# Kernel tuning notes

Measured on AMD Instinct MI355X. Metric: run time of the kernel, lower is better.

Reference implementation:

```python
import jax, jax.numpy as jnp
import numpy as np
from jax import lax

NEG = -1e9  # finite stand-in for -inf (keeps gradients NaN-free)
EPS = 1e-7  # keras.backend.epsilon()


def _logadd3(a, b, c):
    m = jnp.maximum(jnp.maximum(a, b), c)
    return m + jnp.log(jnp.exp(a - m) + jnp.exp(b - m) + jnp.exp(c - m))


def setup_inputs() -> dict:
    key = jax.random.key(0)
    k1, k2, k3, k4 = jax.random.split(key, 4)
    B, T, V, L = 32, 1000, 1024, 100
    logits = jax.random.normal(k1, (B, T, V), dtype=jnp.float32)
    predictions = jax.nn.softmax(logits, axis=-1)  # ctc_batch_cost expects probabilities
    labels = jax.random.randint(k2, (B, L), 0, V - 1, dtype=jnp.int32)  # blank=V-1 excluded
    input_lengths = jax.random.randint(k3, (B, 1), T // 2, T + 1, dtype=jnp.int32)
    label_lengths = jax.random.randint(k4, (B, 1), L // 2, L + 1, dtype=jnp.int32)
    return {"predictions": predictions, "input_lengths": input_lengths,
            "labels": labels, "label_lengths": label_lengths}


def _ctc_loss(predictions, input_lengths, labels, label_lengths):
    B, T, V = predictions.shape
    L = labels.shape[1]
    S = 2 * L + 1
    blank = V - 1

    log_probs = jnp.log(predictions + EPS)  # [B,T,V]

    # Extended label sequence: blank interleaved -> [B,S]
    ext = jnp.full((B, S), blank, dtype=jnp.int32).at[:, 1::2].set(labels)
    ext_m2 = jnp.concatenate([jnp.full((B, 2), -1, jnp.int32), ext[:, :-2]], axis=1)
    allow_skip = (ext != blank) & (ext != ext_m2)  # [B,S]

    s_idx = jnp.arange(S)[None, :]
    valid = s_idx < (2 * label_lengths + 1)  # [B,S] mask of reachable DP lanes

    # Emission log-probs along the extended sequence: [B,T,S]
    emit = jnp.take_along_axis(log_probs, jnp.broadcast_to(ext[:, None, :], (B, T, S)), axis=2)

    alpha0 = jnp.full((B, S), NEG, dtype=log_probs.dtype)
    alpha0 = alpha0.at[:, 0].set(emit[:, 0, 0]).at[:, 1].set(emit[:, 0, 1])
    alpha0 = jnp.where(valid, alpha0, NEG)

    neg1 = jnp.full((B, 1), NEG, dtype=log_probs.dtype)
    neg2 = jnp.full((B, 2), NEG, dtype=log_probs.dtype)

    def step(alpha, xs):
        emit_t, t = xs
        a = alpha
        b = jnp.concatenate([neg1, alpha[:, :-1]], axis=1)
        c = jnp.where(allow_skip, jnp.concatenate([neg2, alpha[:, :-2]], axis=1), NEG)
        new = jnp.where(valid, _logadd3(a, b, c) + emit_t, NEG)
        alpha = jnp.where(t < input_lengths, new, alpha)  # freeze past input_length
        return alpha, None

    emits = jnp.swapaxes(emit, 0, 1)[1:]  # [T-1,B,S]
    ts = jnp.arange(1, T)
    alpha_final, _ = lax.scan(step, alpha0, (emits, ts))

    a_lab = jnp.take_along_axis(alpha_final, 2 * label_lengths - 1, axis=1)  # last label
    a_blk = jnp.take_along_axis(alpha_final, 2 * label_lengths, axis=1)      # trailing blank
    loglik = jnp.logaddexp(a_lab, a_blk)  # [B,1]
    return -loglik


def reference(predictions, input_lengths, labels, label_lengths):
    per_utt = _ctc_loss(predictions, input_lengths, labels, label_lengths)  # [B,1]
    return jnp.mean(per_utt)
```

## Files before the change

kernel.cpp:

```cpp
#include <hip/hip_runtime.h>

#define EPSF  (1e-7f)
#define LN2F  (0.69314718055994530942f)

constexpr int Tc = 1000;
constexpr int Vc = 1024;
constexpr int Lc = 100;
constexpr int GW = 128;
constexpr int CH = 32;

#define SHFLUP1Z(x) __int_as_float(__builtin_amdgcn_update_dpp( \
        0, __float_as_int(x), 0x138, 0xF, 0xF, false))

#define DPPMAXSTEP(x, ctrl) \
    x = fmaxf(x, __int_as_float(__builtin_amdgcn_update_dpp( \
        0, __float_as_int(x), ctrl, 0xF, 0xF, true)))

__global__ __launch_bounds__(128) void ctc_gather_kernel(
    const float* __restrict__ pred,
    const int*   __restrict__ labels,
    const int*   __restrict__ ilen,
    float*       __restrict__ E)
{
    const int row = blockIdx.x;
    const int j   = threadIdx.x;
    const int b   = row / Tc;
    const int t   = row - b * Tc;
    if (t >= ilen[b]) return;
    const int* lab = labels + b * Lc;
    int col = -1;
    if (j < 64) {
        if (j < 50)       col = lab[2 * j];
        else if (j == 50) col = Vc - 1;
    } else {
        int k = j - 64;
        if (k < 50)       col = lab[2 * k + 1];
    }
    float v = 0.0f;
    if (col >= 0) v = pred[(size_t)row * Vc + col] + EPSF;
    E[(size_t)row * GW + j] = v;
}

__global__ __launch_bounds__(64) void ctc_dp_kernel(
    const float* __restrict__ E,
    const int*   __restrict__ ilen,
    const int*   __restrict__ labels,
    const int*   __restrict__ llen,
    float*       __restrict__ loss)
{
    const int b = blockIdx.x;
    const int l = threadIdx.x;

    const int il = ilen[b];
    const int ll = llen[b];
    const int Tb = min(Tc, il);

    const int* lab = labels + b * Lc;
    const int lab0 = lab[min(2 * l,     Lc - 1)];
    const int lab1 = lab[min(2 * l + 1, Lc - 1)];
    const int labm = lab[max(2 * l - 1, 0)];
    const bool allow1 = (l == 0) || (lab0 != labm);
    const bool allow3 = (lab1 != lab0);

    const int Sv = 2 * ll + 1;
    const bool valid0 = (4 * l + 0) < Sv;
    const bool valid1 = (4 * l + 1) < Sv;
    const bool valid2 = (4 * l + 2) < Sv;
    const bool valid3 = (4 * l + 3) < Sv;

    const float* Eb = E + (size_t)b * Tc * GW;

    __shared__ float lds[2][CH][GW];
    __shared__ float sh[256];

    float a0 = 0.0f, a1 = 0.0f, a2 = 0.0f, a3 = 0.0f;
    if (l == 0) { a0 = Eb[50]; a1 = Eb[0]; }
    int Eshift = 0;

#define STEP(Lb, r) do {                                                      \
        float e0_ = (Lb)[(r) * GW + l];                                       \
        float e1_ = (Lb)[(r) * GW + 64 + l];                                  \
        float eb_ = (Lb)[(r) * GW + 50];                                      \
        float p3s_ = SHFLUP1Z(a3);                                            \
        float p2s_ = SHFLUP1Z(a2);                                            \
        float n0_ = (a0 + p3s_) * eb_;                                        \
        float c1_ = allow1 ? p2s_ : 0.0f;                                     \
        float n1_ = (a1 + a0 + c1_) * e0_;                                    \
        float n2_ = (a2 + a1) * eb_;                                          \
        float c3_ = allow3 ? a1 : 0.0f;                                       \
        float n3_ = (a3 + a2 + c3_) * e1_;                                    \
        a0 = valid0 ? n0_ : 0.0f;                                             \
        a1 = valid1 ? n1_ : 0.0f;                                             \
        a2 = valid2 ? n2_ : 0.0f;                                             \
        a3 = valid3 ? n3_ : 0.0f;                                             \
    } while (0)

#define RESCALE() do {                                                        \
        float m_ = fmaxf(fmaxf(a0, a1), fmaxf(a2, a3));                       \
        DPPMAXSTEP(m_, 0x111);                                \
        DPPMAXSTEP(m_, 0x112);                                \
        DPPMAXSTEP(m_, 0x114);                                \
        DPPMAXSTEP(m_, 0x118);                                \
        DPPMAXSTEP(m_, 0x142);                              \
        DPPMAXSTEP(m_, 0x143);                              \
        int mb_ = __builtin_amdgcn_readlane(__float_as_int(m_), 63);          \
        int Ee_ = (mb_ >> 23) & 0xFF;                                         \
        float sc_ = __int_as_float((253 - Ee_) << 23);        \
        a0 *= sc_; a1 *= sc_; a2 *= sc_; a3 *= sc_;                           \
        Eshift += Ee_ - 126;                                                  \
    } while (0)

#define LOADCHUNK(t0n_) do {                                                  \
        _Pragma("unroll")                                                     \
        for (int p_ = 0; p_ < 16; ++p_) {                                     \
            int r0_ = min((t0n_) + 2 * p_, Tc - 2);                           \
            g[p_] = *(const float4*)(Eb + (size_t)r0_ * GW + 4 * l);          \
        }                                                                     \
    } while (0)

#define WRITECHUNK(buf_) do {                                                 \
        float* d_ = &lds[buf_][0][0] + 4 * l;                                 \
        _Pragma("unroll")                                                     \
        for (int p_ = 0; p_ < 16; ++p_) {                                     \
            *(float4*)(d_ + p_ * 2 * GW) = g[p_];                             \
        }                                                                     \
    } while (0)

    float4 g[16];

    LOADCHUNK(0);
    __builtin_amdgcn_sched_barrier(0);
    WRITECHUNK(0);
    int buf = 0;

    {
        const bool pf = (CH < Tb);
        if (pf) LOADCHUNK(CH);
        __builtin_amdgcn_sched_barrier(0);
        const float* Lb = &lds[0][0][0];
#pragma unroll
        for (int k = 1; k < 8; ++k) STEP(Lb, k);
        RESCALE();
#pragma unroll
        for (int gi = 1; gi < 4; ++gi) {
#pragma unroll
            for (int k = 0; k < 8; ++k) STEP(Lb, gi * 8 + k);
            RESCALE();
        }
        if (pf) WRITECHUNK(1);
        buf = 1;
    }

    for (int t0 = CH; t0 < Tb; t0 += CH) {
        const int t0n = t0 + CH;
        const bool pf = (t0n < Tb);
        if (pf) LOADCHUNK(t0n);
        __builtin_amdgcn_sched_barrier(0);
        const float* Lb = &lds[buf][0][0];
        const int ns = min(CH, Tb - t0);
        if (ns == CH) {
#pragma unroll
            for (int gi = 0; gi < 4; ++gi) {
#pragma unroll
                for (int k = 0; k < 8; ++k) STEP(Lb, gi * 8 + k);
                RESCALE();
            }
        } else {
            for (int r = 0; r < ns; ++r) {
                STEP(Lb, r);
                if ((r & 7) == 7) RESCALE();
            }
        }
        if (pf) WRITECHUNK(buf ^ 1);
        buf ^= 1;
    }
#undef STEP
#undef RESCALE
#undef LOADCHUNK
#undef WRITECHUNK

    sh[4 * l + 0] = a0; sh[4 * l + 1] = a1;
    sh[4 * l + 2] = a2; sh[4 * l + 3] = a3;
    __syncthreads();
    if (l == 0) {
        float x = sh[2 * ll - 1], y = sh[2 * ll];
        loss[b] = -(__logf(x + y) + (float)Eshift * LN2F);
    }
}

__global__ void ctc_reduce_kernel(const float* __restrict__ loss,
                                  float* __restrict__ out, int B)
{
    int lane = threadIdx.x;
    float x = (lane < B) ? loss[lane] : 0.0f;
#pragma unroll
    for (int off = 32; off > 0; off >>= 1)
        x += __shfl_down(x, off);
    if (lane == 0) out[0] = x / (float)B;
}

extern "C" void kernel_launch(void* const* d_in, const int* in_sizes, int n_in,
                              void* d_out, int out_size, void* d_ws, size_t ws_size,
                              hipStream_t stream)
{
    const float* pred   = (const float*)d_in[0];
    const int*   ilen   = (const int*)d_in[1];
    const int*   labels = (const int*)d_in[2];
    const int*   llen   = (const int*)d_in[3];
    float*       out    = (float*)d_out;
    float*       wsloss = (float*)d_ws;
    float*       Ebuf   = (float*)((char*)d_ws + 256);

    const int B = in_sizes[1];

    ctc_gather_kernel<<<B * Tc, 128, 0, stream>>>(pred, labels, ilen, Ebuf);
    ctc_dp_kernel<<<B, 64, 0, stream>>>(Ebuf, ilen, labels, llen, wsloss);
    ctc_reduce_kernel<<<1, 64, 0, stream>>>(wsloss, out, B);
}
```

Baseline: 270.3 us.

## Prefetch DP emissions into registers and fold validity masks into gather

The DP kernel no longer stages emission rows through a double-buffered LDS chunk. Each lane now loads its own emission values directly from global memory into register arrays, grouped eight rows at a time and issued 32 time steps ahead of use. The per-step validity selects are removed: the gather kernel writes zero emissions for label lanes beyond the label length, so unreachable states stay at zero on their own. The skip gating becomes an FMA with a 0/1 multiplier. This removes LDS writes, reads and per-step selects from the serial recurrence, at the cost of higher register use and reliance on global load latency being hidden by the prefetch distance.

```diff
diff --git a/kernel.cpp b/kernel.cpp
--- a/kernel.cpp
+++ b/kernel.cpp
@@ -7,7 +7,6 @@
 constexpr int Vc = 1024;
 constexpr int Lc = 100;
 constexpr int GW = 128;
-constexpr int CH = 32;
 
 #define SHFLUP1Z(x) __int_as_float(__builtin_amdgcn_update_dpp( \
         0, __float_as_int(x), 0x138, 0xF, 0xF, false))
@@ -20,6 +19,7 @@
     const float* __restrict__ pred,
     const int*   __restrict__ labels,
     const int*   __restrict__ ilen,
+    const int*   __restrict__ llen,
     float*       __restrict__ E)
 {
     const int row = blockIdx.x;
@@ -27,17 +27,20 @@
     const int b   = row / Tc;
     const int t   = row - b * Tc;
     if (t >= ilen[b]) return;
+    const int ll = llen[b];
     const int* lab = labels + b * Lc;
-    int col = -1;
+    float v = 0.0f;
     if (j < 64) {
-        if (j < 50)       col = lab[2 * j];
-        else if (j == 50) col = Vc - 1;
+        if (j < 50) {
+            if (2 * j < ll) v = pred[(size_t)row * Vc + lab[2 * j]] + EPSF;
+        } else if (j == 50) {
+            v = pred[(size_t)row * Vc + (Vc - 1)] + EPSF;
+        }
     } else {
         int k = j - 64;
-        if (k < 50)       col = lab[2 * k + 1];
-    }
-    float v = 0.0f;
-    if (col >= 0) v = pred[(size_t)row * Vc + col] + EPSF;
+        if (k < 50 && (2 * k + 1) < ll)
+            v = pred[(size_t)row * Vc + lab[2 * k + 1]] + EPSF;
+    }
     E[(size_t)row * GW + j] = v;
 }
 
@@ -59,40 +62,52 @@
     const int lab0 = lab[min(2 * l,     Lc - 1)];
     const int lab1 = lab[min(2 * l + 1, Lc - 1)];
     const int labm = lab[max(2 * l - 1, 0)];
-    const bool allow1 = (l == 0) || (lab0 != labm);
-    const bool allow3 = (lab1 != lab0);
-
-    const int Sv = 2 * ll + 1;
-    const bool valid0 = (4 * l + 0) < Sv;
-    const bool valid1 = (4 * l + 1) < Sv;
-    const bool valid2 = (4 * l + 2) < Sv;
-    const bool valid3 = (4 * l + 3) < Sv;
+    const float allow1f = ((l == 0) || (lab0 != labm)) ? 1.0f : 0.0f;
+    const float allow3f = (lab1 != lab0) ? 1.0f : 0.0f;
 
     const float* Eb = E + (size_t)b * Tc * GW;
 
-    __shared__ float lds[2][CH][GW];
     __shared__ float sh[256];
 
     float a0 = 0.0f, a1 = 0.0f, a2 = 0.0f, a3 = 0.0f;
     if (l == 0) { a0 = Eb[50]; a1 = Eb[0]; }
     int Eshift = 0;
 
-#define STEP(Lb, r) do {                                                      \
-        float e0_ = (Lb)[(r) * GW + l];                                       \
-        float e1_ = (Lb)[(r) * GW + 64 + l];                                  \
-        float eb_ = (Lb)[(r) * GW + 50];                                      \
+    float v0[32], v1[32], vb[32];
+
+#define LOADG(gi, baseRow) do {                                               \
+        const int br_ = (baseRow);                                            \
+        if (br_ + 7 <= Tc - 1) {                                              \
+            const float* p_ = Eb + (size_t)br_ * GW;                          \
+            _Pragma("unroll")                                                 \
+            for (int k_ = 0; k_ < 8; ++k_) {                                  \
+                v0[8 * (gi) + k_] = p_[k_ * GW + l];                          \
+                v1[8 * (gi) + k_] = p_[k_ * GW + 64 + l];                     \
+                vb[8 * (gi) + k_] = p_[k_ * GW + 50];                         \
+            }                                                                 \
+        } else {                                                              \
+            _Pragma("unroll")                                                 \
+            for (int k_ = 0; k_ < 8; ++k_) {                                  \
+                int r_ = min(br_ + k_, Tc - 1);    \
+                const float* p_ = Eb + (size_t)r_ * GW;                       \
+                v0[8 * (gi) + k_] = p_[l];                                    \
+                v1[8 * (gi) + k_] = p_[64 + l];                               \
+                vb[8 * (gi) + k_] = p_[50];                                   \
+            }                                                                 \
+        }                                                                     \
+    } while (0)
+
+#define STEP(gi, k) do {                                                      \
+        float e0_ = v0[8 * (gi) + (k)];                                       \
+        float e1_ = v1[8 * (gi) + (k)];                                       \
+        float eb_ = vb[8 * (gi) + (k)];                                       \
         float p3s_ = SHFLUP1Z(a3);                                            \
         float p2s_ = SHFLUP1Z(a2);                                            \
         float n0_ = (a0 + p3s_) * eb_;                                        \
-        float c1_ = allow1 ? p2s_ : 0.0f;                                     \
-        float n1_ = (a1 + a0 + c1_) * e0_;                                    \
+        float n1_ = fmaf(p2s_, allow1f, a1 + a0) * e0_;                       \
         float n2_ = (a2 + a1) * eb_;                                          \
-        float c3_ = allow3 ? a1 : 0.0f;                                       \
-        float n3_ = (a3 + a2 + c3_) * e1_;                                    \
-        a0 = valid0 ? n0_ : 0.0f;                                             \
-        a1 = valid1 ? n1_ : 0.0f;                                             \
-        a2 = valid2 ? n2_ : 0.0f;                                             \
-        a3 = valid3 ? n3_ : 0.0f;                                             \
+        float n3_ = fmaf(a1, allow3f, a3 + a2) * e1_;                         \
+        a0 = n0_; a1 = n1_; a2 = n2_; a3 = n3_;                               \
     } while (0)
 
 #define RESCALE() do {                                                        \
@@ -110,74 +125,44 @@
         Eshift += Ee_ - 126;                                                  \
     } while (0)
 
-#define LOADCHUNK(t0n_) do {                                                  \
-        _Pragma("unroll")                                                     \
-        for (int p_ = 0; p_ < 16; ++p_) {                                     \
-            int r0_ = min((t0n_) + 2 * p_, Tc - 2);                           \
-            g[p_] = *(const float4*)(Eb + (size_t)r0_ * GW + 4 * l);          \
-        }                                                                     \
-    } while (0)
-
-#define WRITECHUNK(buf_) do {                                                 \
-        float* d_ = &lds[buf_][0][0] + 4 * l;                                 \
-        _Pragma("unroll")                                                     \
-        for (int p_ = 0; p_ < 16; ++p_) {                                     \
-            *(float4*)(d_ + p_ * 2 * GW) = g[p_];                             \
-        }                                                                     \
-    } while (0)
-
-    float4 g[16];
-
-    LOADCHUNK(0);
-    __builtin_amdgcn_sched_barrier(0);
-    WRITECHUNK(0);
-    int buf = 0;
-
-    {
-        const bool pf = (CH < Tb);
-        if (pf) LOADCHUNK(CH);
-        __builtin_amdgcn_sched_barrier(0);
-        const float* Lb = &lds[0][0][0];
-#pragma unroll
-        for (int k = 1; k < 8; ++k) STEP(Lb, k);
-        RESCALE();
-#pragma unroll
-        for (int gi = 1; gi < 4; ++gi) {
-#pragma unroll
-            for (int k = 0; k < 8; ++k) STEP(Lb, gi * 8 + k);
-            RESCALE();
+    LOADG(0, 1); LOADG(1, 9); LOADG(2, 17); LOADG(3, 25);
+
+    int t0 = 1;
+    for (; t0 + 32 <= Tb; t0 += 32) {
+        __builtin_amdgcn_sched_barrier(0);
+#pragma unroll
+        for (int k = 0; k < 8; ++k) STEP(0, k);
+        RESCALE();
+        LOADG(0, t0 + 32);
+        __builtin_amdgcn_sched_barrier(0);
+#pragma unroll
+        for (int k = 0; k < 8; ++k) STEP(1, k);
+        RESCALE();
+        LOADG(1, t0 + 40);
+        __builtin_amdgcn_sched_barrier(0);
+#pragma unroll
+        for (int k = 0; k < 8; ++k) STEP(2, k);
+        RESCALE();
+        LOADG(2, t0 + 48);
+        __builtin_amdgcn_sched_barrier(0);
+#pragma unroll
+        for (int k = 0; k < 8; ++k) STEP(3, k);
+        RESCALE();
+        LOADG(3, t0 + 56);
+    }
+
+#pragma unroll
+    for (int g = 0; g < 4; ++g) {
+        __builtin_amdgcn_sched_barrier(0);
+#pragma unroll
+        for (int k = 0; k < 8; ++k) {
+            if (t0 + 8 * g + k < Tb) STEP(g, k);
         }
-        if (pf) WRITECHUNK(1);
-        buf = 1;
-    }
-
-    for (int t0 = CH; t0 < Tb; t0 += CH) {
-        const int t0n = t0 + CH;
-        const bool pf = (t0n < Tb);
-        if (pf) LOADCHUNK(t0n);
-        __builtin_amdgcn_sched_barrier(0);
-        const float* Lb = &lds[buf][0][0];
-        const int ns = min(CH, Tb - t0);
-        if (ns == CH) {
-#pragma unroll
-            for (int gi = 0; gi < 4; ++gi) {
-#pragma unroll
-                for (int k = 0; k < 8; ++k) STEP(Lb, gi * 8 + k);
-                RESCALE();
-            }
-        } else {
-            for (int r = 0; r < ns; ++r) {
-                STEP(Lb, r);
-                if ((r & 7) == 7) RESCALE();
-            }
-        }
-        if (pf) WRITECHUNK(buf ^ 1);
-        buf ^= 1;
-    }
+        RESCALE();
+    }
+#undef LOADG
 #undef STEP
 #undef RESCALE
-#undef LOADCHUNK
-#undef WRITECHUNK
 
     sh[4 * l + 0] = a0; sh[4 * l + 1] = a1;
     sh[4 * l + 2] = a2; sh[4 * l + 3] = a3;
@@ -213,7 +198,7 @@
 
     const int B = in_sizes[1];
 
-    ctc_gather_kernel<<<B * Tc, 128, 0, stream>>>(pred, labels, ilen, Ebuf);
+    ctc_gather_kernel<<<B * Tc, 128, 0, stream>>>(pred, labels, ilen, llen, Ebuf);
     ctc_dp_kernel<<<B, 64, 0, stream>>>(Ebuf, ilen, labels, llen, wsloss);
     ctc_reduce_kernel<<<1, 64, 0, stream>>>(wsloss, out, B);
 }
```

After: 260.4 us. 1.04x faster.
